# Optimization experiments

Measured on AMD Instinct MI355X. Metric: run time of the kernel, lower is better.

Reference implementation:

```python
import jax, jax.numpy as jnp
import numpy as np

B, S = 2, 2048
HQ, HKV, D = 32, 8, 128
SCALING = 0.08838834764831845  # 1/sqrt(128)
E4M3_MAX = 448.0
FP4_MAX = 6.0
# e2m1 representable magnitudes and decision midpoints
FP4_GRID = jnp.array([0.0, 0.5, 1.0, 1.5, 2.0, 3.0, 4.0, 6.0], dtype=jnp.float32)
FP4_MID = (FP4_GRID[:-1] + FP4_GRID[1:]) / 2.0


def quant_dequant_e4m3(x):
    """Simulate torch .to(float8_e4m3fn): clamp to +-448, round mantissa to 3 bits."""
    ax = jnp.abs(x)
    xc = jnp.clip(x, -E4M3_MAX, E4M3_MAX)
    e = jnp.clip(jnp.floor(jnp.log2(jnp.maximum(ax, 1e-12))), -6.0, 8.0)
    q = jnp.round(xc * jnp.exp2(3.0 - e)) * jnp.exp2(e - 3.0)
    return jnp.where(ax == 0.0, 0.0, q)


def quant_dequant_fp4(x):
    """FP4 (e2m1) compress/decompress with per-(token,head) absmax scale over head_dim.
    x: [B, S, H, D] -> dequantized [B, S, H, D]."""
    scale = jnp.max(jnp.abs(x), axis=-1, keepdims=True) / FP4_MAX  # [B,S,H,1]
    scale = jnp.maximum(scale, 1e-12)
    xn = x / scale
    idx = jnp.searchsorted(FP4_MID, jnp.abs(xn))  # nearest e2m1 magnitude
    return jnp.sign(xn) * FP4_GRID[idx] * scale


def setup_inputs() -> dict:
    key = jax.random.key(0)
    kq, kk, kv = jax.random.split(key, 3)
    q = jax.random.normal(kq, (B, S, HQ * D), dtype=jnp.float32)
    k = jax.random.normal(kk, (B, S, HKV * D), dtype=jnp.float32)
    v = jax.random.normal(kv, (B, S, HKV * D), dtype=jnp.float32)
    return {"q": q, "k": k, "v": v}


def reference(q, k, v):
    # reshape to heads
    qh = q.reshape(B, S, HQ, D)
    kh = k.reshape(B, S, HKV, D)
    vh = v.reshape(B, S, HKV, D)
    # FP8 cast then FP4 compress/decompress of the KV cache
    kq8 = quant_dequant_e4m3(kh)
    vq8 = quant_dequant_e4m3(vh)
    kd = quant_dequant_fp4(kq8)
    vd = quant_dequant_fp4(vq8)
    # GQA: expand kv heads to query heads
    g = HQ // HKV
    kr = jnp.repeat(kd, g, axis=2)  # [B,S,HQ,D]
    vr = jnp.repeat(vd, g, axis=2)
    scores = jnp.einsum("bqhd,bkhd->bhqk", qh, kr) * SCALING  # [B,HQ,S,S]
    causal = jnp.tril(jnp.ones((S, S), dtype=bool))
    scores = jnp.where(causal[None, None], scores, jnp.float32(-1e30))
    probs = jax.nn.softmax(scores, axis=-1)
    out = jnp.einsum("bhqk,bkhd->bqhd", probs, vr)
    return out.reshape(B, S, HQ * D)
```

## Files before the change

kernel.cpp:

```cpp
#include <hip/hip_runtime.h>
#include <cstdint>
#include <cstddef>

#define B_    2
#define S_    2048
#define HQ_   32
#define HKV_  8
#define D_    128
#define QSCALE_ (0.08838834764831845f * 1.4426950408889634f)

#define NROW_ (B_*S_*HKV_)

typedef __bf16 bf16x8 __attribute__((ext_vector_type(8)));
typedef float  f32x4  __attribute__((ext_vector_type(4)));

__device__ __forceinline__ unsigned short f2bfu(float f) {
    __bf16 b = (__bf16)f;
    return __builtin_bit_cast(unsigned short, b);
}

__device__ __forceinline__ void gl_lds16(const unsigned short* g, unsigned short* l) {
    __builtin_amdgcn_global_load_lds(
        (const __attribute__((address_space(1))) void*)g,
        (__attribute__((address_space(3))) void*)l, 16, 0, 0);
}

__device__ __forceinline__ float qd_e4m3(float x) {
    float ax = fabsf(x);
    float xc = fminf(fmaxf(x, -448.f), 448.f);
    float axc = fmaxf(ax, 1e-12f);
    int e = (int)((__builtin_bit_cast(unsigned int, axc) >> 23) & 255u) - 127;
    e = min(max(e, -6), 8);
    float s1 = __builtin_bit_cast(float, (unsigned int)(130 - e) << 23);
    float s2 = __builtin_bit_cast(float, (unsigned int)(124 + e) << 23);
    float q = rintf(xc * s1) * s2;
    return ax == 0.f ? 0.f : q;
}

__device__ __forceinline__ float qd_fp4(float x, float scale) {
    float xn = x / scale;
    float a = fabsf(xn);
    float g;
    if      (a <= 0.25f) g = 0.f;
    else if (a <= 0.75f) g = 0.5f;
    else if (a <= 1.25f) g = 1.f;
    else if (a <= 1.75f) g = 1.5f;
    else if (a <= 2.5f)  g = 2.f;
    else if (a <= 3.5f)  g = 3.f;
    else if (a <= 5.f)   g = 4.f;
    else                 g = 6.f;
    return copysignf(g * scale, xn);
}

__global__ __launch_bounds__(256) void prep(const float* __restrict__ k,
                                            const float* __restrict__ v,
                                            unsigned short* __restrict__ kd,
                                            unsigned short* __restrict__ vdT) {
    __shared__ alignas(16) unsigned short t[64][136];
    if (blockIdx.x < 8192) {
        int gw = (blockIdx.x * 256 + threadIdx.x) >> 6;
        int lane = threadIdx.x & 63;
        int row = gw;
        int b   = row / (S_ * HKV_);
        int rem = row - b * (S_ * HKV_);
        int s   = rem >> 3;
        int h   = rem & 7;
        float2 x = *(const float2*)(k + (size_t)row * D_ + 2 * lane);
        float q0 = qd_e4m3(x.x);
        float q1 = qd_e4m3(x.y);
        float amax = fmaxf(fabsf(q0), fabsf(q1));
#pragma unroll
        for (int m = 1; m < 64; m <<= 1) amax = fmaxf(amax, __shfl_xor(amax, m, 64));
        float scale = fmaxf(amax / 6.0f, 1e-12f);
        float y0 = qd_fp4(q0, scale);
        float y1 = qd_fp4(q1, scale);
        size_t outOff = ((size_t)(b * HKV_ + h) * S_ + s) * D_ + 2 * lane;
        unsigned int pack = (unsigned int)f2bfu(y0) | ((unsigned int)f2bfu(y1) << 16);
        *(unsigned int*)(kd + outOff) = pack;
    } else {
        int bid = blockIdx.x - 8192;
        int bh = bid >> 5;
        int st = bid & 31;
        int s0 = st * 64;
        int b = bh >> 3;
        int h = bh & 7;
        int tid = threadIdx.x;
        int lane = tid & 63;
        int wave = tid >> 6;
#pragma unroll
        for (int i = 0; i < 8; ++i) {
            int rA = wave * 16 + 2 * i;
            const float* srcA = v + (((size_t)b * S_ + (s0 + rA)) * HKV_ + h) * D_ + 2 * lane;
            const float* srcB = srcA + (size_t)HKV_ * D_;
            float2 xA = *(const float2*)srcA;
            float2 xB = *(const float2*)srcB;
            float a0 = qd_e4m3(xA.x), a1 = qd_e4m3(xA.y);
            float c0 = qd_e4m3(xB.x), c1 = qd_e4m3(xB.y);
            float amA = fmaxf(fabsf(a0), fabsf(a1));
            float amB = fmaxf(fabsf(c0), fabsf(c1));
#pragma unroll
            for (int m = 1; m < 64; m <<= 1) {
                amA = fmaxf(amA, __shfl_xor(amA, m, 64));
                amB = fmaxf(amB, __shfl_xor(amB, m, 64));
            }
            float sA = fmaxf(amA / 6.0f, 1e-12f);
            float sB = fmaxf(amB / 6.0f, 1e-12f);
            unsigned int pA = (unsigned int)f2bfu(qd_fp4(a0, sA)) |
                              ((unsigned int)f2bfu(qd_fp4(a1, sA)) << 16);
            unsigned int pB = (unsigned int)f2bfu(qd_fp4(c0, sB)) |
                              ((unsigned int)f2bfu(qd_fp4(c1, sB)) << 16);
            *(unsigned int*)&t[rA][2 * lane]     = pA;
            *(unsigned int*)&t[rA + 1][2 * lane] = pB;
        }
        __syncthreads();
        int d = tid >> 1;
        unsigned short* dp = vdT + ((size_t)bh * D_ + d) * S_ + s0;
#pragma unroll
        for (int i = 0; i < 4; ++i) {
            int c = (tid & 1) + 2 * i;
            int so = c * 8;
            unsigned short tmp[8];
#pragma unroll
            for (int e = 0; e < 8; ++e) tmp[e] = t[so + e][d];
            *(uint4*)(dp + so) = *(uint4*)tmp;
        }
    }
}

__global__ __launch_bounds__(256) void attn(const float* __restrict__ q,
                                            const unsigned short* __restrict__ kd,
                                            const unsigned short* __restrict__ vdT,
                                            float* __restrict__ out) {
    int bh = blockIdx.x;
    int yp = blockIdx.y;
    int b  = bh >> 5;
    int hq = bh & 31;
    int hkv = hq >> 2;
    int tid  = threadIdx.x;
    int lane = tid & 63;
    int wave = tid >> 6;
    int m16  = lane & 15;
    int g    = lane >> 4;
    int m8   = m16 & 7;

    __shared__ alignas(16) unsigned short ks[64 * 128];
    __shared__ alignas(16) unsigned short vs[128 * 64];
    __shared__ alignas(16) unsigned short ps[4 * 16 * 64];

    const unsigned short* kbase = kd  + (size_t)(b * HKV_ + hkv) * S_ * D_;
    const unsigned short* vbase = vdT + (size_t)(b * HKV_ + hkv) * D_ * S_;

    bf16x8 vones;
#pragma unroll
    for (int j = 0; j < 8; ++j) vones[j] = (__bf16)1.0f;

    for (int phase = 0; phase < 2; ++phase) {
        int qt = phase ? yp : (31 - yp);
        int q0 = qt * 64;
        int qrowBase = q0 + wave * 16;

        bf16x8 qf[4];
        const float* qp = q + (((size_t)b * S_ + (qrowBase + m16)) * HQ_ + hq) * D_;
#pragma unroll
        for (int c = 0; c < 4; ++c) {
            const float* p0 = qp + c * 32 + g * 8;
            bf16x8 f;
#pragma unroll
            for (int j = 0; j < 8; ++j) f[j] = (__bf16)(p0[j] * QSCALE_);
            qf[c] = f;
        }

        f32x4 o[8];
#pragma unroll
        for (int i = 0; i < 8; ++i) o[i] = (f32x4){0.f, 0.f, 0.f, 0.f};
        f32x4 o9 = (f32x4){0.f, 0.f, 0.f, 0.f};

        for (int kt = 0; kt <= qt; ++kt) {
            int k0 = kt * 64;
            __syncthreads();
#pragma unroll
            for (int i = 0; i < 4; ++i) {
                int row = wave * 16 + i * 4 + (lane >> 4);
                int c = (lane & 15) ^ (row & 15);
                gl_lds16(kbase + (size_t)(k0 + row) * D_ + c * 8,
                         &ks[wave * 2048 + i * 512]);
            }
#pragma unroll
            for (int i = 0; i < 4; ++i) {
                int d = wave * 32 + i * 8 + (lane >> 3);
                int c = (lane & 7) ^ (d & 7);
                gl_lds16(vbase + (size_t)d * S_ + k0 + c * 8,
                         &vs[wave * 2048 + i * 512]);
            }
            __syncthreads();

            bool diag = (kt == qt);
            int kcmax = diag ? ((wave >> 1) + 1) : 2;

            f32x4 sacc[4];
#pragma unroll
            for (int n = 0; n < 4; ++n) sacc[n] = (f32x4){0.f, 0.f, 0.f, 0.f};
            __builtin_amdgcn_s_setprio(1);
#pragma unroll
            for (int n = 0; n < 4; ++n) {
                if (!diag || n <= wave) {
#pragma unroll
                    for (int c = 0; c < 4; ++c) {
                        bf16x8 ak = *(const bf16x8*)&ks[(n * 16 + m16) * 128 +
                                                        (((c * 4 + g) ^ m16) * 8)];
                        sacc[n] = __builtin_amdgcn_mfma_f32_16x16x32_bf16(ak, qf[c], sacc[n], 0, 0, 0);
                    }
                }
            }
            __builtin_amdgcn_s_setprio(0);

            int qloc = wave * 16 + m16;
            float pv[4][4];
#pragma unroll
            for (int n = 0; n < 4; ++n) {
                if (!diag || n <= wave) {
#pragma unroll
                    for (int r = 0; r < 4; ++r) {
                        float p = exp2f(sacc[n][r]);
                        if (diag) {
                            int key = n * 16 + g * 4 + r;
                            p = (key <= qloc) ? p : 0.f;
                        }
                        pv[n][r] = p;
                    }
                }
            }

#pragma unroll
            for (int n = 0; n < 4; ++n) {
                if (n < 2 * kcmax) {
                    unsigned int lo = 0, hi = 0;
                    if (!diag || n <= wave) {
                        lo = (unsigned int)f2bfu(pv[n][0]) | ((unsigned int)f2bfu(pv[n][1]) << 16);
                        hi = (unsigned int)f2bfu(pv[n][2]) | ((unsigned int)f2bfu(pv[n][3]) << 16);
                    }
                    int chunk = (n * 2 + (g >> 1)) ^ m8;
                    uint2 val; val.x = lo; val.y = hi;
                    *(uint2*)&ps[wave * 1024 + m16 * 64 + chunk * 8 + (g & 1) * 4] = val;
                }
            }
            asm volatile("s_waitcnt lgkmcnt(0)" ::: "memory");

            __builtin_amdgcn_s_setprio(1);
#pragma unroll
            for (int kc = 0; kc < 2; ++kc) {
                if (kc < kcmax) {
                    bf16x8 pa = *(const bf16x8*)&ps[wave * 1024 + m16 * 64 +
                                                    (((kc * 4 + g) ^ m8) * 8)];
                    o9 = __builtin_amdgcn_mfma_f32_16x16x32_bf16(pa, vones, o9, 0, 0, 0);
#pragma unroll
                    for (int ds = 0; ds < 8; ++ds) {
                        bf16x8 vb = *(const bf16x8*)&vs[(ds * 16 + m16) * 64 +
                                                        (((kc * 4 + g) ^ m8) * 8)];
                        o[ds] = __builtin_amdgcn_mfma_f32_16x16x32_bf16(pa, vb, o[ds], 0, 0, 0);
                    }
                }
            }
            __builtin_amdgcn_s_setprio(0);
        }

#pragma unroll
        for (int r = 0; r < 4; ++r) {
            float inv = 1.f / o9[r];
            float* op = out + (((size_t)b * S_ + (qrowBase + g * 4 + r)) * HQ_ + hq) * D_;
#pragma unroll
            for (int ds = 0; ds < 8; ++ds)
                op[ds * 16 + m16] = o[ds][r] * inv;
        }
    }
}

extern "C" void kernel_launch(void* const* d_in, const int* in_sizes, int n_in,
                              void* d_out, int out_size, void* d_ws, size_t ws_size,
                              hipStream_t stream) {
    const float* q = (const float*)d_in[0];
    const float* k = (const float*)d_in[1];
    const float* v = (const float*)d_in[2];
    float* out = (float*)d_out;

    unsigned short* kd  = (unsigned short*)d_ws;
    unsigned short* vdT = kd + (size_t)NROW_ * D_;

    prep<<<8704, 256, 0, stream>>>(k, v, kd, vdT);
    attn<<<dim3(64, 16), 256, 0, stream>>>(q, kd, vdT, out);
}
```

Baseline: 259.6 us.

## Transpose P in registers with permlane swaps and drop paired-tile scheduling

The P tile is no longer staged through LDS. The score accumulator layout is converted to the MFMA A-operand layout in registers using permlane32_swap and permlane16_swap, which removes the LDS writes, the waitcnt and the reads per key tile. Each block now handles a single query tile, with the grid doubled to 32 in y, instead of pairing a long tile with a short one for balance. This adds more blocks with uneven causal work and relies on the gfx950 permlane swap instructions.

```diff
diff --git a/kernel.cpp b/kernel.cpp
--- a/kernel.cpp
+++ b/kernel.cpp
@@ -13,10 +13,11 @@
 
 typedef __bf16 bf16x8 __attribute__((ext_vector_type(8)));
 typedef float  f32x4  __attribute__((ext_vector_type(4)));
-
-__device__ __forceinline__ unsigned short f2bfu(float f) {
+typedef unsigned int u32x4 __attribute__((ext_vector_type(4)));
+
+__device__ __forceinline__ unsigned int f2bfu(float f) {
     __bf16 b = (__bf16)f;
-    return __builtin_bit_cast(unsigned short, b);
+    return (unsigned int)__builtin_bit_cast(unsigned short, b);
 }
 
 __device__ __forceinline__ void gl_lds16(const unsigned short* g, unsigned short* l) {
@@ -75,7 +76,7 @@
         float y0 = qd_fp4(q0, scale);
         float y1 = qd_fp4(q1, scale);
         size_t outOff = ((size_t)(b * HKV_ + h) * S_ + s) * D_ + 2 * lane;
-        unsigned int pack = (unsigned int)f2bfu(y0) | ((unsigned int)f2bfu(y1) << 16);
+        unsigned int pack = f2bfu(y0) | (f2bfu(y1) << 16);
         *(unsigned int*)(kd + outOff) = pack;
     } else {
         int bid = blockIdx.x - 8192;
@@ -105,10 +106,8 @@
             }
             float sA = fmaxf(amA / 6.0f, 1e-12f);
             float sB = fmaxf(amB / 6.0f, 1e-12f);
-            unsigned int pA = (unsigned int)f2bfu(qd_fp4(a0, sA)) |
-                              ((unsigned int)f2bfu(qd_fp4(a1, sA)) << 16);
-            unsigned int pB = (unsigned int)f2bfu(qd_fp4(c0, sB)) |
-                              ((unsigned int)f2bfu(qd_fp4(c1, sB)) << 16);
+            unsigned int pA = f2bfu(qd_fp4(a0, sA)) | (f2bfu(qd_fp4(a1, sA)) << 16);
+            unsigned int pB = f2bfu(qd_fp4(c0, sB)) | (f2bfu(qd_fp4(c1, sB)) << 16);
             *(unsigned int*)&t[rA][2 * lane]     = pA;
             *(unsigned int*)&t[rA + 1][2 * lane] = pB;
         }
@@ -132,7 +131,7 @@
                                             const unsigned short* __restrict__ vdT,
                                             float* __restrict__ out) {
     int bh = blockIdx.x;
-    int yp = blockIdx.y;
+    int qt = 31 - blockIdx.y;
     int b  = bh >> 5;
     int hq = bh & 31;
     int hkv = hq >> 2;
@@ -145,7 +144,6 @@
 
     __shared__ alignas(16) unsigned short ks[64 * 128];
     __shared__ alignas(16) unsigned short vs[128 * 64];
-    __shared__ alignas(16) unsigned short ps[4 * 16 * 64];
 
     const unsigned short* kbase = kd  + (size_t)(b * HKV_ + hkv) * S_ * D_;
     const unsigned short* vbase = vdT + (size_t)(b * HKV_ + hkv) * D_ * S_;
@@ -154,124 +152,115 @@
 #pragma unroll
     for (int j = 0; j < 8; ++j) vones[j] = (__bf16)1.0f;
 
-    for (int phase = 0; phase < 2; ++phase) {
-        int qt = phase ? yp : (31 - yp);
-        int q0 = qt * 64;
-        int qrowBase = q0 + wave * 16;
-
-        bf16x8 qf[4];
-        const float* qp = q + (((size_t)b * S_ + (qrowBase + m16)) * HQ_ + hq) * D_;
-#pragma unroll
-        for (int c = 0; c < 4; ++c) {
-            const float* p0 = qp + c * 32 + g * 8;
-            bf16x8 f;
-#pragma unroll
-            for (int j = 0; j < 8; ++j) f[j] = (__bf16)(p0[j] * QSCALE_);
-            qf[c] = f;
-        }
-
-        f32x4 o[8];
-#pragma unroll
-        for (int i = 0; i < 8; ++i) o[i] = (f32x4){0.f, 0.f, 0.f, 0.f};
-        f32x4 o9 = (f32x4){0.f, 0.f, 0.f, 0.f};
-
-        for (int kt = 0; kt <= qt; ++kt) {
-            int k0 = kt * 64;
-            __syncthreads();
-#pragma unroll
-            for (int i = 0; i < 4; ++i) {
-                int row = wave * 16 + i * 4 + (lane >> 4);
-                int c = (lane & 15) ^ (row & 15);
-                gl_lds16(kbase + (size_t)(k0 + row) * D_ + c * 8,
-                         &ks[wave * 2048 + i * 512]);
-            }
-#pragma unroll
-            for (int i = 0; i < 4; ++i) {
-                int d = wave * 32 + i * 8 + (lane >> 3);
-                int c = (lane & 7) ^ (d & 7);
-                gl_lds16(vbase + (size_t)d * S_ + k0 + c * 8,
-                         &vs[wave * 2048 + i * 512]);
-            }
-            __syncthreads();
-
-            bool diag = (kt == qt);
-            int kcmax = diag ? ((wave >> 1) + 1) : 2;
-
-            f32x4 sacc[4];
-#pragma unroll
-            for (int n = 0; n < 4; ++n) sacc[n] = (f32x4){0.f, 0.f, 0.f, 0.f};
-            __builtin_amdgcn_s_setprio(1);
-#pragma unroll
-            for (int n = 0; n < 4; ++n) {
-                if (!diag || n <= wave) {
-#pragma unroll
-                    for (int c = 0; c < 4; ++c) {
-                        bf16x8 ak = *(const bf16x8*)&ks[(n * 16 + m16) * 128 +
-                                                        (((c * 4 + g) ^ m16) * 8)];
-                        sacc[n] = __builtin_amdgcn_mfma_f32_16x16x32_bf16(ak, qf[c], sacc[n], 0, 0, 0);
+    int q0 = qt * 64;
+    int qrowBase = q0 + wave * 16;
+
+    bf16x8 qf[4];
+    const float* qp = q + (((size_t)b * S_ + (qrowBase + m16)) * HQ_ + hq) * D_;
+#pragma unroll
+    for (int c = 0; c < 4; ++c) {
+        const float* p0 = qp + c * 32 + g * 8;
+        bf16x8 f;
+#pragma unroll
+        for (int j = 0; j < 8; ++j) f[j] = (__bf16)(p0[j] * QSCALE_);
+        qf[c] = f;
+    }
+
+    f32x4 o[8];
+#pragma unroll
+    for (int i = 0; i < 8; ++i) o[i] = (f32x4){0.f, 0.f, 0.f, 0.f};
+    f32x4 o9 = (f32x4){0.f, 0.f, 0.f, 0.f};
+
+    for (int kt = 0; kt <= qt; ++kt) {
+        int k0 = kt * 64;
+        __syncthreads();
+#pragma unroll
+        for (int i = 0; i < 4; ++i) {
+            int row = wave * 16 + i * 4 + (lane >> 4);
+            int c = (lane & 15) ^ (row & 15);
+            gl_lds16(kbase + (size_t)(k0 + row) * D_ + c * 8,
+                     &ks[wave * 2048 + i * 512]);
+        }
+#pragma unroll
+        for (int i = 0; i < 4; ++i) {
+            int d = wave * 32 + i * 8 + (lane >> 3);
+            int c = (lane & 7) ^ (d & 7);
+            gl_lds16(vbase + (size_t)d * S_ + k0 + c * 8,
+                     &vs[wave * 2048 + i * 512]);
+        }
+        __syncthreads();
+
+        bool diag = (kt == qt);
+        int kcmax = diag ? ((wave >> 1) + 1) : 2;
+
+        f32x4 sacc[4];
+#pragma unroll
+        for (int n = 0; n < 4; ++n) sacc[n] = (f32x4){0.f, 0.f, 0.f, 0.f};
+        __builtin_amdgcn_s_setprio(1);
+#pragma unroll
+        for (int n = 0; n < 4; ++n) {
+            if (!diag || n <= wave) {
+#pragma unroll
+                for (int c = 0; c < 4; ++c) {
+                    bf16x8 ak = *(const bf16x8*)&ks[(n * 16 + m16) * 128 +
+                                                    (((c * 4 + g) ^ m16) * 8)];
+                    sacc[n] = __builtin_amdgcn_mfma_f32_16x16x32_bf16(ak, qf[c], sacc[n], 0, 0, 0);
+                }
+            }
+        }
+        __builtin_amdgcn_s_setprio(0);
+
+        int qloc = wave * 16 + m16;
+        unsigned int Dlo[4], Dhi[4];
+#pragma unroll
+        for (int n = 0; n < 4; ++n) {
+            if (!diag || n <= wave) {
+                float pr[4];
+#pragma unroll
+                for (int r = 0; r < 4; ++r) {
+                    float p = exp2f(sacc[n][r]);
+                    if (diag) {
+                        int key = n * 16 + g * 4 + r;
+                        p = (key <= qloc) ? p : 0.f;
                     }
+                    pr[r] = p;
                 }
-            }
-            __builtin_amdgcn_s_setprio(0);
-
-            int qloc = wave * 16 + m16;
-            float pv[4][4];
-#pragma unroll
-            for (int n = 0; n < 4; ++n) {
-                if (!diag || n <= wave) {
-#pragma unroll
-                    for (int r = 0; r < 4; ++r) {
-                        float p = exp2f(sacc[n][r]);
-                        if (diag) {
-                            int key = n * 16 + g * 4 + r;
-                            p = (key <= qloc) ? p : 0.f;
-                        }
-                        pv[n][r] = p;
-                    }
+                Dlo[n] = f2bfu(pr[0]) | (f2bfu(pr[1]) << 16);
+                Dhi[n] = f2bfu(pr[2]) | (f2bfu(pr[3]) << 16);
+            } else {
+                Dlo[n] = 0u; Dhi[n] = 0u;
+            }
+        }
+
+        __builtin_amdgcn_s_setprio(1);
+#pragma unroll
+        for (int kc = 0; kc < 2; ++kc) {
+            if (kc < kcmax) {
+                auto p0 = __builtin_amdgcn_permlane32_swap(Dlo[2 * kc], Dlo[2 * kc + 1], false, false);
+                auto p1 = __builtin_amdgcn_permlane32_swap(Dhi[2 * kc], Dhi[2 * kc + 1], false, false);
+                auto r0 = __builtin_amdgcn_permlane16_swap(p0[0], p0[1], false, false);
+                auto r1 = __builtin_amdgcn_permlane16_swap(p1[0], p1[1], false, false);
+                u32x4 pau = (u32x4){r0[0], r1[0], r0[1], r1[1]};
+                bf16x8 pa = __builtin_bit_cast(bf16x8, pau);
+                o9 = __builtin_amdgcn_mfma_f32_16x16x32_bf16(pa, vones, o9, 0, 0, 0);
+#pragma unroll
+                for (int ds = 0; ds < 8; ++ds) {
+                    bf16x8 vb = *(const bf16x8*)&vs[(ds * 16 + m16) * 64 +
+                                                    (((kc * 4 + g) ^ m8) * 8)];
+                    o[ds] = __builtin_amdgcn_mfma_f32_16x16x32_bf16(pa, vb, o[ds], 0, 0, 0);
                 }
             }
-
-#pragma unroll
-            for (int n = 0; n < 4; ++n) {
-                if (n < 2 * kcmax) {
-                    unsigned int lo = 0, hi = 0;
-                    if (!diag || n <= wave) {
-                        lo = (unsigned int)f2bfu(pv[n][0]) | ((unsigned int)f2bfu(pv[n][1]) << 16);
-                        hi = (unsigned int)f2bfu(pv[n][2]) | ((unsigned int)f2bfu(pv[n][3]) << 16);
-                    }
-                    int chunk = (n * 2 + (g >> 1)) ^ m8;
-                    uint2 val; val.x = lo; val.y = hi;
-                    *(uint2*)&ps[wave * 1024 + m16 * 64 + chunk * 8 + (g & 1) * 4] = val;
-                }
-            }
-            asm volatile("s_waitcnt lgkmcnt(0)" ::: "memory");
-
-            __builtin_amdgcn_s_setprio(1);
-#pragma unroll
-            for (int kc = 0; kc < 2; ++kc) {
-                if (kc < kcmax) {
-                    bf16x8 pa = *(const bf16x8*)&ps[wave * 1024 + m16 * 64 +
-                                                    (((kc * 4 + g) ^ m8) * 8)];
-                    o9 = __builtin_amdgcn_mfma_f32_16x16x32_bf16(pa, vones, o9, 0, 0, 0);
-#pragma unroll
-                    for (int ds = 0; ds < 8; ++ds) {
-                        bf16x8 vb = *(const bf16x8*)&vs[(ds * 16 + m16) * 64 +
-                                                        (((kc * 4 + g) ^ m8) * 8)];
-                        o[ds] = __builtin_amdgcn_mfma_f32_16x16x32_bf16(pa, vb, o[ds], 0, 0, 0);
-                    }
-                }
-            }
-            __builtin_amdgcn_s_setprio(0);
-        }
-
-#pragma unroll
-        for (int r = 0; r < 4; ++r) {
-            float inv = 1.f / o9[r];
-            float* op = out + (((size_t)b * S_ + (qrowBase + g * 4 + r)) * HQ_ + hq) * D_;
-#pragma unroll
-            for (int ds = 0; ds < 8; ++ds)
-                op[ds * 16 + m16] = o[ds][r] * inv;
-        }
+        }
+        __builtin_amdgcn_s_setprio(0);
+    }
+
+#pragma unroll
+    for (int r = 0; r < 4; ++r) {
+        float inv = 1.f / o9[r];
+        float* op = out + (((size_t)b * S_ + (qrowBase + g * 4 + r)) * HQ_ + hq) * D_;
+#pragma unroll
+        for (int ds = 0; ds < 8; ++ds)
+            op[ds * 16 + m16] = o[ds][r] * inv;
     }
 }
 
@@ -287,5 +276,5 @@
     unsigned short* vdT = kd + (size_t)NROW_ * D_;
 
     prep<<<8704, 256, 0, stream>>>(k, v, kd, vdT);
-    attn<<<dim3(64, 16), 256, 0, stream>>>(q, kd, vdT, out);
-}
+    attn<<<dim3(64, 32), 256, 0, stream>>>(q, kd, vdT, out);
+}
```

New measurement: 255.4 us. About the same (-1.6%).
